# Performance work log

Hardware: AMD Instinct MI355X
Metric: run time of the kernel (lower is better)

Reference implementation:

```python
import jax, jax.numpy as jnp
import numpy as np

DIM = 256
HEADS = 8


def setup_inputs() -> dict:
    key = jax.random.key(0)
    ks = jax.random.split(key, 12)
    B, N, L, C, H = 2, 1024, 4096, DIM, HEADS
    s = C ** -0.5
    inp = {
        "query": jax.random.normal(ks[0], (B, N, C), jnp.float32),
        "key": jax.random.normal(ks[1], (B, L, C), jnp.float32),
        "value": jax.random.normal(ks[2], (B, L, C), jnp.float32),
        "key_padding_mask": jnp.zeros((B, L), jnp.bool_),
        "hw_lvl": 1,
        # nn.Linear weights, stored as (out, in) like torch
        "Wq": jax.random.normal(ks[3], (C, C), jnp.float32) * s,
        "Wk": jax.random.normal(ks[4], (C, C), jnp.float32) * s,
        "Wv": jax.random.normal(ks[5], (C, C), jnp.float32) * s,
        "Wp": jax.random.normal(ks[6], (C, C), jnp.float32) * s,
        "bp": jax.random.normal(ks[7], (C,), jnp.float32) * 0.02,
        "W1": jax.random.normal(ks[8], (H, H), jnp.float32) * H ** -0.5,
        "b1": jax.random.normal(ks[9], (H,), jnp.float32) * 0.02,
        "W2": jax.random.normal(ks[10], (1, H), jnp.float32) * H ** -0.5,
        "b2": jax.random.normal(ks[11], (1,), jnp.float32) * 0.02,
    }
    return inp


def reference(query, key, value, key_padding_mask, hw_lvl,
              Wq, Wk, Wv, Wp, bp, W1, b1, W2, b2):
    # key_padding_mask and hw_lvl are accepted but unused by the original module.
    B, N, C = query.shape
    L = key.shape[1]
    H = W1.shape[0]
    D = C // H
    scale = D ** -0.5

    q = (query @ Wq.T).reshape(B, N, H, D)  # bnhd
    k = (key @ Wk.T).reshape(B, L, H, D)    # blhd
    v = (value @ Wv.T).reshape(B, L, H, D)  # blhd

    # raw attention scores [B, H, N, L]
    attn = jnp.einsum("bnhd,blhd->bhnl", q, k) * scale

    # per-score tiny MLP over the head axis -> mask [B, N, L, 1]
    scores_nlh = attn.transpose(0, 2, 3, 1)  # [B, N, L, H]
    new_feats = jax.nn.relu(scores_nlh @ W1.T + b1)
    mask = jax.nn.relu(new_feats @ W2.T + b2)  # [B, N, L, 1]

    a = jax.nn.softmax(attn, axis=-1)  # dropout p=0 -> identity
    x = jnp.einsum("bhnl,blhd->bnhd", a, v).reshape(B, N, C)
    x = x @ Wp.T + bp
    return x, mask
```

## Files before the change

kernel.cpp:

```cpp
#include <hip/hip_runtime.h>

typedef unsigned short u16;
typedef unsigned int u32;
typedef __attribute__((ext_vector_type(8))) short bf16x8;
typedef __attribute__((ext_vector_type(4))) short bf16x4;
typedef __attribute__((ext_vector_type(4))) float f32x4;
typedef __attribute__((ext_vector_type(2))) float f32x2;

#define QK_SCALE 0.17677669529663687f

__device__ inline float bf2f(u16 h) {
    u32 u = ((u32)h) << 16; float f; __builtin_memcpy(&f, &u, 4); return f;
}
__device__ inline u16 f2bf(float f) {
    u32 u; __builtin_memcpy(&u, &f, 4);
    u = u + 0x7fffu + ((u >> 16) & 1u);
    return (u16)(u >> 16);
}

__global__ __launch_bounds__(256) void cvt_all_kernel(
    const float* __restrict__ q, const float* __restrict__ k,
    const float* __restrict__ v,
    const float* __restrict__ Wq, const float* __restrict__ Wk,
    const float* __restrict__ Wv, const float* __restrict__ Wp,
    u16* __restrict__ qf, u16* __restrict__ kf, u16* __restrict__ vf,
    u16* __restrict__ wqb, u16* __restrict__ wkb, u16* __restrict__ wvb,
    u16* __restrict__ wpb)
{
    const int bx = blockIdx.x;
    const float* src; u16* dst; int base;
    if (bx < 256)       { src = q;  dst = qf;  base = bx; }
    else if (bx < 1280) { src = k;  dst = kf;  base = bx - 256; }
    else if (bx < 2304) { src = v;  dst = vf;  base = bx - 1280; }
    else if (bx < 2336) { src = Wq; dst = wqb; base = bx - 2304; }
    else if (bx < 2368) { src = Wk; dst = wkb; base = bx - 2336; }
    else if (bx < 2400) { src = Wv; dst = wvb; base = bx - 2368; }
    else                { src = Wp; dst = wpb; base = bx - 2400; }
    const int i = base * 2048 + threadIdx.x * 8;
    const f32x4 a = *(const f32x4*)(src + i);
    const f32x4 b = *(const f32x4*)(src + i + 4);
    bf16x8 o;
#pragma unroll
    for (int j = 0; j < 4; ++j) {
        o[j]     = (short)f2bf(a[j]);
        o[j + 4] = (short)f2bf(b[j]);
    }
    *(bf16x8*)(dst + i) = o;
}

__global__ __launch_bounds__(256) void proj_kernel(
    const u16* __restrict__ qf, const u16* __restrict__ kf,
    const u16* __restrict__ vf,
    const u16* __restrict__ wqb, const u16* __restrict__ wkb,
    const u16* __restrict__ wvb,
    u16* __restrict__ qb, u16* __restrict__ kb, u16* __restrict__ vt)
{
    const int bx = blockIdx.x;
    const u16 *X, *W; u16* outb; int m0, mode;
    if (bx < 128)      { X = qf; W = wqb; outb = qb; m0 = bx * 16; mode = 2; }
    else if (bx < 640) { X = kf; W = wkb; outb = kb; m0 = (bx - 128) * 16; mode = 0; }
    else               { X = vf; W = wvb; outb = vt; m0 = (bx - 640) * 16; mode = 1; }

    const int lane = threadIdx.x & 63;
    const int w = threadIdx.x >> 6;
    const int r = lane & 15, g = lane >> 4;
    const int c0 = blockIdx.y * 64 + w * 16;
    const u16* ap = X + (long)(m0 + r) * 256 + g * 8;
    const u16* bp = W + (long)(c0 + r) * 256 + g * 8;

    bf16x8 af[8], bf[8];
#pragma unroll
    for (int ks = 0; ks < 8; ++ks) af[ks] = *(const bf16x8*)(ap + ks * 32);
#pragma unroll
    for (int ks = 0; ks < 8; ++ks) bf[ks] = *(const bf16x8*)(bp + ks * 32);

    f32x4 acc = {0.f, 0.f, 0.f, 0.f};
#pragma unroll
    for (int ks = 0; ks < 8; ++ks)
        acc = __builtin_amdgcn_mfma_f32_16x16x32_bf16(af[ks], bf[ks], acc, 0, 0, 0);

    const int c = c0 + r;
    if (mode == 1) {
        const int m_ = m0 + g * 4;
        const int b = m_ >> 12, l = m_ & 4095;
        bf16x4 pk;
#pragma unroll
        for (int j = 0; j < 4; ++j) pk[j] = (short)f2bf(acc[j]);
        *(bf16x4*)(vt + (long)b * 1048576 + (long)(l >> 2) * 1024 + c * 4) = pk;
    } else {
#pragma unroll
        for (int j = 0; j < 4; ++j) {
            const int m = m0 + g * 4 + j;
            if (mode == 2) outb[(long)m * 256 + c] = f2bf(acc[j] * QK_SCALE);
            else           outb[(long)m * 256 + c] = f2bf(acc[j]);
        }
    }
}

__global__ __launch_bounds__(256, 2) void attn_split_kernel(
    const u16* __restrict__ qb, const u16* __restrict__ kb,
    const u16* __restrict__ vt,
    const float* __restrict__ W1, const float* __restrict__ b1,
    const float* __restrict__ W2, const float* __restrict__ b2,
    u16* __restrict__ Opart, float* __restrict__ stats,
    float* __restrict__ out)
{
    __shared__ float ored[4][8][2][2][16][4];
    __shared__ float rs[4][8][16];

    const int tid = threadIdx.x;
    const int w = tid >> 6, lane = tid & 63;
    const int r = lane & 15, g = lane >> 4;
    const int bi = blockIdx.y;
    const int n0 = blockIdx.x * 16;
    const int cz = blockIdx.z;

    float w1r[64], b1r[8], w2r[8];
#pragma unroll
    for (int i = 0; i < 64; ++i) w1r[i] = W1[i];
#pragma unroll
    for (int i = 0; i < 8; ++i) { b1r[i] = b1[i]; w2r[i] = W2[i]; }
    const float b2r = b2[0];

    bf16x8 qh[8];
    const long qbase = (long)(bi * 1024 + n0 + r) * 256 + g * 8;
#pragma unroll
    for (int h = 0; h < 8; ++h)
        qh[h] = *(const bf16x8*)(qb + qbase + h * 32);

    f32x4 oacc[8][2];
#pragma unroll
    for (int h = 0; h < 8; ++h)
#pragma unroll
        for (int c = 0; c < 2; ++c) oacc[h][c] = (f32x4){0.f, 0.f, 0.f, 0.f};
    float rsum[8];
#pragma unroll
    for (int h = 0; h < 8; ++h) rsum[h] = 0.f;

    bf16x8 kf[8];
    {
        const long kbb = (long)(bi * 4096 + cz * 512 + w * 16 + r) * 256 + g * 8;
#pragma unroll
        for (int h = 0; h < 8; ++h)
            kf[h] = *(const bf16x8*)(kb + kbb + h * 32);
    }

    for (int t = 0; t < 8; ++t) {
        const int l0 = cz * 512 + t * 64;

        f32x4 ss[8];
#pragma unroll
        for (int h = 0; h < 8; ++h) {
            f32x4 z = {0.f, 0.f, 0.f, 0.f};
            ss[h] = __builtin_amdgcn_mfma_f32_16x16x32_bf16(kf[h], qh[h], z, 0, 0, 0);
        }

        if (t < 7) {
            const long kbb = (long)(bi * 4096 + l0 + 64 + w * 16 + r) * 256 + g * 8;
#pragma unroll
            for (int h = 0; h < 8; ++h)
                kf[h] = *(const bf16x8*)(kb + kbb + h * 32);
        }

        {
            f32x4 mv4;
#pragma unroll
            for (int jp = 0; jp < 2; ++jp) {
                f32x2 mv = {b2r, b2r};
#pragma unroll
                for (int f = 0; f < 8; ++f) {
                    f32x2 ft = {b1r[f], b1r[f]};
#pragma unroll
                    for (int h = 0; h < 8; ++h) {
                        const float wv = w1r[f * 8 + h];
                        const f32x2 s2 = {ss[h][jp * 2], ss[h][jp * 2 + 1]};
                        ft = __builtin_elementwise_fma(s2, (f32x2){wv, wv}, ft);
                    }
                    ft = __builtin_elementwise_max(ft, (f32x2){0.f, 0.f});
                    mv = __builtin_elementwise_fma(ft, (f32x2){w2r[f], w2r[f]}, mv);
                }
                mv = __builtin_elementwise_max(mv, (f32x2){0.f, 0.f});
                mv4[jp * 2]     = mv[0];
                mv4[jp * 2 + 1] = mv[1];
            }
            *(f32x4*)(out + 524288l + (long)(bi * 1024 + n0 + r) * 4096
                      + l0 + w * 16 + g * 4) = mv4;
        }

        bf16x4 vf[8][2];
        {
            const u16* vb = vt + (long)bi * 1048576 +
                            (long)((l0 >> 2) + w * 4 + g) * 1024;
#pragma unroll
            for (int h = 0; h < 8; ++h)
#pragma unroll
                for (int c = 0; c < 2; ++c)
                    vf[h][c] = *(const bf16x4*)(vb + (h * 32 + c * 16 + r) * 4);
        }

        bf16x4 pa[8];
#pragma unroll
        for (int h = 0; h < 8; ++h) {
            float e0 = __expf(ss[h][0] - 8.f);
            float e1 = __expf(ss[h][1] - 8.f);
            float e2 = __expf(ss[h][2] - 8.f);
            float e3 = __expf(ss[h][3] - 8.f);
            rsum[h] += (e0 + e1) + (e2 + e3);
            u32 u0, u1, u2, u3;
            __builtin_memcpy(&u0, &e0, 4); __builtin_memcpy(&u1, &e1, 4);
            __builtin_memcpy(&u2, &e2, 4); __builtin_memcpy(&u3, &e3, 4);
            u32 lohi[2];
            lohi[0] = (u0 >> 16) | (u1 & 0xFFFF0000u);
            lohi[1] = (u2 >> 16) | (u3 & 0xFFFF0000u);
            __builtin_memcpy(&pa[h], lohi, 8);
        }

#pragma unroll
        for (int h = 0; h < 8; ++h)
#pragma unroll
            for (int c = 0; c < 2; ++c)
                oacc[h][c] = __builtin_amdgcn_mfma_f32_16x16x16bf16_1k(
                    pa[h], vf[h][c], oacc[h][c], 0, 0, 0);
    }

#pragma unroll
    for (int h = 0; h < 8; ++h) {
        float v = rsum[h];
        v += __shfl_xor(v, 16);
        v += __shfl_xor(v, 32);
        if (g == 0) rs[w][h][r] = v;
    }
#pragma unroll
    for (int ph = 0; ph < 2; ++ph) {
        if ((g >> 1) == ph) {
#pragma unroll
            for (int h = 0; h < 8; ++h)
#pragma unroll
                for (int c = 0; c < 2; ++c)
                    *(f32x4*)&ored[w][h][c][g & 1][r][0] = oacc[h][c];
        }
        __syncthreads();
        if (ph == 0 && tid < 128) {
            const int h = tid >> 4, n = tid & 15;
            stats[((long)(bi * 8 + cz) * 8 + h) * 1024 + n0 + n] =
                rs[0][h][n] + rs[1][h][n] + rs[2][h][n] + rs[3][h][n];
        }
        {
            const int h = tid >> 5, c = (tid >> 4) & 1, rr = tid & 15;
#pragma unroll
            for (int g2 = 0; g2 < 2; ++g2)
#pragma unroll
                for (int j = 0; j < 4; ++j) {
                    const float val =
                        ored[0][h][c][g2][rr][j] + ored[1][h][c][g2][rr][j] +
                        ored[2][h][c][g2][rr][j] + ored[3][h][c][g2][rr][j];
                    const int n = (ph * 2 + g2) * 4 + j;
                    Opart[((long)(bi * 8 + cz) * 1024 + n0 + n) * 256
                          + h * 32 + c * 16 + rr] = f2bf(val);
                }
        }
        if (ph == 0) __syncthreads();
    }
}

__global__ __launch_bounds__(512) void reduce_kernel(
    const u16* __restrict__ Opart, const float* __restrict__ stats,
    const u16* __restrict__ wpb, const float* __restrict__ bp,
    float* __restrict__ out)
{
    __shared__ __align__(16) u16 xt[16 * 272];
    const int tid = threadIdx.x;
    const int bi = blockIdx.y, n0 = blockIdx.x * 16, bz = blockIdx.z;

    {
        const int n = tid >> 5, cg = tid & 31, h = cg >> 2;
        float S = 0.f, O[8];
#pragma unroll
        for (int k = 0; k < 8; ++k) O[k] = 0.f;
#pragma unroll
        for (int c = 0; c < 8; ++c) {
            S += stats[((long)(bi * 8 + c) * 8 + h) * 1024 + n0 + n];
            bf16x8 v0 = *(const bf16x8*)(Opart +
                ((long)(bi * 8 + c) * 1024 + n0 + n) * 256 + cg * 8);
#pragma unroll
            for (int k = 0; k < 8; ++k) O[k] += bf2f((u16)v0[k]);
        }
        const float inv = 1.f / S;
        bf16x8 pk;
#pragma unroll
        for (int k = 0; k < 8; ++k) pk[k] = (short)f2bf(O[k] * inv);
        *(bf16x8*)(&xt[n * 272 + cg * 8]) = pk;
    }
    __syncthreads();

    const int w = tid >> 6, lane = tid & 63;
    const int r = lane & 15, g = lane >> 4;
    bf16x8 a8[8];
#pragma unroll
    for (int ks = 0; ks < 8; ++ks)
        a8[ks] = *(const bf16x8*)(&xt[r * 272 + ks * 32 + g * 8]);
    const int cp0 = (bz * 8 + w) * 16;
    f32x4 acc = {0.f, 0.f, 0.f, 0.f};
#pragma unroll
    for (int ks = 0; ks < 8; ++ks) {
        bf16x8 wb = *(const bf16x8*)(wpb + (long)(cp0 + r) * 256 + ks * 32 + g * 8);
        acc = __builtin_amdgcn_mfma_f32_16x16x32_bf16(a8[ks], wb, acc, 0, 0, 0);
    }
    const int cp = cp0 + r;
    const float bpv = bp[cp];
#pragma unroll
    for (int j = 0; j < 4; ++j) {
        const int nn = g * 4 + j;
        out[(long)(bi * 1024 + n0 + nn) * 256 + cp] = acc[j] + bpv;
    }
}

extern "C" void kernel_launch(void* const* d_in, const int* in_sizes, int n_in,
                              void* d_out, int out_size, void* d_ws, size_t ws_size,
                              hipStream_t stream)
{
    const float* query = (const float*)d_in[0];
    const float* key   = (const float*)d_in[1];
    const float* value = (const float*)d_in[2];
    const float* Wq = (const float*)d_in[5];
    const float* Wk = (const float*)d_in[6];
    const float* Wv = (const float*)d_in[7];
    const float* Wp = (const float*)d_in[8];
    const float* bp = (const float*)d_in[9];
    const float* W1 = (const float*)d_in[10];
    const float* b1 = (const float*)d_in[11];
    const float* W2 = (const float*)d_in[12];
    const float* b2 = (const float*)d_in[13];

    u16* qb    = (u16*)d_ws;
    u16* kb    = qb + 524288;
    u16* vtp   = kb + 2097152;
    u16* wpb   = vtp + 2097152;
    u16* Opart = wpb + 65536;
    u16* kfb   = Opart;
    u16* vfb   = Opart + 2097152;
    float* stats = (float*)(Opart + 4194304);
    u16* qfb   = (u16*)(stats + 131072);
    u16* wqb   = qfb + 524288;
    u16* wkb   = wqb + 65536;
    u16* wvb   = wkb + 65536;
    float* out = (float*)d_out;

    cvt_all_kernel<<<2432, 256, 0, stream>>>(
        query, key, value, Wq, Wk, Wv, Wp,
        qfb, kfb, vfb, wqb, wkb, wvb, wpb);
    proj_kernel<<<dim3(1152, 4), 256, 0, stream>>>(
        qfb, kfb, vfb, wqb, wkb, wvb, qb, kb, vtp);
    attn_split_kernel<<<dim3(64, 2, 8), 256, 0, stream>>>(
        qb, kb, vtp, W1, b1, W2, b2, Opart, stats, out);
    reduce_kernel<<<dim3(64, 2, 2), 512, 0, stream>>>(Opart, stats, wpb, bp, out);
}
```

Before: 124.7 us.

## Software-pipeline QK MFMA one tile ahead and scalarize mask MLP

Computes the QK score MFMAs for the next 64-key tile before the PV MFMAs of the current tile, and prefetches K two tiles ahead. The goal is to hide MFMA latency and K load latency behind the mask MLP, exp and PV work. It also fully unrolls the tile loop and replaces the packed f32x2 mask MLP with scalar fmaf. The cost is higher register pressure, since the score registers stay live across iterations, which could reduce occupancy.

```diff
diff --git a/kernel.cpp b/kernel.cpp
--- a/kernel.cpp
+++ b/kernel.cpp
@@ -5,7 +5,6 @@
 typedef __attribute__((ext_vector_type(8))) short bf16x8;
 typedef __attribute__((ext_vector_type(4))) short bf16x4;
 typedef __attribute__((ext_vector_type(4))) float f32x4;
-typedef __attribute__((ext_vector_type(2))) float f32x2;
 
 #define QK_SCALE 0.17677669529663687f
 
@@ -138,50 +137,44 @@
     for (int h = 0; h < 8; ++h) rsum[h] = 0.f;
 
     bf16x8 kf[8];
+    f32x4 ss[8];
+
     {
         const long kbb = (long)(bi * 4096 + cz * 512 + w * 16 + r) * 256 + g * 8;
 #pragma unroll
         for (int h = 0; h < 8; ++h)
             kf[h] = *(const bf16x8*)(kb + kbb + h * 32);
     }
-
+#pragma unroll
+    for (int h = 0; h < 8; ++h) {
+        f32x4 z = {0.f, 0.f, 0.f, 0.f};
+        ss[h] = __builtin_amdgcn_mfma_f32_16x16x32_bf16(kf[h], qh[h], z, 0, 0, 0);
+    }
+    {
+        const long kbb = (long)(bi * 4096 + cz * 512 + 64 + w * 16 + r) * 256 + g * 8;
+#pragma unroll
+        for (int h = 0; h < 8; ++h)
+            kf[h] = *(const bf16x8*)(kb + kbb + h * 32);
+    }
+
+#pragma unroll
     for (int t = 0; t < 8; ++t) {
         const int l0 = cz * 512 + t * 64;
 
-        f32x4 ss[8];
-#pragma unroll
-        for (int h = 0; h < 8; ++h) {
-            f32x4 z = {0.f, 0.f, 0.f, 0.f};
-            ss[h] = __builtin_amdgcn_mfma_f32_16x16x32_bf16(kf[h], qh[h], z, 0, 0, 0);
-        }
-
-        if (t < 7) {
-            const long kbb = (long)(bi * 4096 + l0 + 64 + w * 16 + r) * 256 + g * 8;
-#pragma unroll
-            for (int h = 0; h < 8; ++h)
-                kf[h] = *(const bf16x8*)(kb + kbb + h * 32);
-        }
-
         {
             f32x4 mv4;
 #pragma unroll
-            for (int jp = 0; jp < 2; ++jp) {
-                f32x2 mv = {b2r, b2r};
+            for (int j = 0; j < 4; ++j) {
+                float mv = b2r;
 #pragma unroll
                 for (int f = 0; f < 8; ++f) {
-                    f32x2 ft = {b1r[f], b1r[f]};
-#pragma unroll
-                    for (int h = 0; h < 8; ++h) {
-                        const float wv = w1r[f * 8 + h];
-                        const f32x2 s2 = {ss[h][jp * 2], ss[h][jp * 2 + 1]};
-                        ft = __builtin_elementwise_fma(s2, (f32x2){wv, wv}, ft);
-                    }
-                    ft = __builtin_elementwise_max(ft, (f32x2){0.f, 0.f});
-                    mv = __builtin_elementwise_fma(ft, (f32x2){w2r[f], w2r[f]}, mv);
+                    float ft = b1r[f];
+#pragma unroll
+                    for (int h = 0; h < 8; ++h)
+                        ft = fmaf(ss[h][j], w1r[f * 8 + h], ft);
+                    mv = fmaf(fmaxf(ft, 0.f), w2r[f], mv);
                 }
-                mv = __builtin_elementwise_max(mv, (f32x2){0.f, 0.f});
-                mv4[jp * 2]     = mv[0];
-                mv4[jp * 2 + 1] = mv[1];
+                mv4[j] = fmaxf(mv, 0.f);
             }
             *(f32x4*)(out + 524288l + (long)(bi * 1024 + n0 + r) * 4096
                       + l0 + w * 16 + g * 4) = mv4;
@@ -215,6 +208,20 @@
             __builtin_memcpy(&pa[h], lohi, 8);
         }
 
+        if (t < 7) {
+#pragma unroll
+            for (int h = 0; h < 8; ++h) {
+                f32x4 z = {0.f, 0.f, 0.f, 0.f};
+                ss[h] = __builtin_amdgcn_mfma_f32_16x16x32_bf16(kf[h], qh[h], z, 0, 0, 0);
+            }
+        }
+        if (t < 6) {
+            const long kbb = (long)(bi * 4096 + l0 + 128 + w * 16 + r) * 256 + g * 8;
+#pragma unroll
+            for (int h = 0; h < 8; ++h)
+                kf[h] = *(const bf16x8*)(kb + kbb + h * 32);
+        }
+
 #pragma unroll
         for (int h = 0; h < 8; ++h)
 #pragma unroll
```

Result: slower. 206.5 us (+65.7%).
